# Kernel optimization log

Measured on AMD Instinct MI355X. Metric: run time of the kernel, lower is better.

Reference implementation:

```python
import jax, jax.numpy as jnp
import numpy as np

BLOCK = 256


def setup_inputs() -> dict:
    key = jax.random.key(0)
    ks = jax.random.split(key, 6)
    b, n, hid = 2, 4096, 2048
    h, d = 16, 128
    x = jax.random.normal(ks[0], (b, n, hid), dtype=jnp.float32)
    slope_rate = jax.random.uniform(ks[1], (h, 1, 1), dtype=jnp.float32)
    Wqkv = jax.random.normal(ks[2], (3 * h * d, hid), dtype=jnp.float32) * 0.02
    Wg = jax.random.normal(ks[3], (h * d, hid), dtype=jnp.float32) * 0.02
    norm_w = jnp.ones((h * d,), dtype=jnp.float32)
    Wo = jax.random.normal(ks[4], (hid, h * d), dtype=jnp.float32) * 0.02
    return {"x": x, "slope_rate": slope_rate, "Wqkv": Wqkv, "Wg": Wg, "norm_w": norm_w, "Wo": Wo}


def reference(x, slope_rate, Wqkv, Wg, norm_w, Wo):
    b, n, hid = x.shape
    h = slope_rate.shape[0]
    d = Wqkv.shape[0] // (3 * h)
    nb = n // BLOCK

    qkv = jax.nn.silu(x @ Wqkv.T).reshape(b, n, h, 3 * d)
    q, k, v = jnp.split(qkv, 3, axis=-1)           # each (b, n, h, d)
    # -> (b, h, n, d)
    q = q.transpose(0, 2, 1, 3)
    k = k.transpose(0, 2, 1, 3)
    v = v.transpose(0, 2, 1, 3)

    s = slope_rate.astype(jnp.float32)             # (h, 1, 1)
    arr = jnp.arange(1, BLOCK + 1, dtype=jnp.float32)
    q_decay = jnp.exp(-s * arr[:, None])           # (h, BLOCK, 1)
    k_decay = jnp.exp(-s * (BLOCK - arr[:, None])) # (h, BLOCK, 1)
    idx = arr[:, None] - arr[None, :]              # (BLOCK, BLOCK)
    diag_decay = jnp.where(idx >= 0, jnp.exp(-s * idx), 0.0)  # (h, BLOCK, BLOCK)
    block_decay = jnp.exp(-s * BLOCK)              # (h, 1, 1)

    # chunk into blocks: (nb, b, h, BLOCK, d)
    def chunk(t):
        return t.reshape(b, h, nb, BLOCK, d).transpose(2, 0, 1, 3, 4)
    qc, kc, vc = chunk(q), chunk(k), chunk(v)

    def step(kv, qkv_blk):
        qi, ki, vi = qkv_blk
        # inter-block: decayed query against running kv state
        out_nd = jnp.einsum('bhmd,bhde->bhme', qi * q_decay, kv)
        # intra-block: decay-masked quadratic attention
        qk = jnp.einsum('bhmd,bhnd->bhmn', qi, ki) * diag_decay
        out_d = jnp.einsum('bhmn,bhne->bhme', qk, vi)
        kv_new = block_decay * kv + jnp.einsum('bhmd,bhme->bhde', ki * k_decay, vi)
        return kv_new, out_nd + out_d

    kv0 = jnp.zeros((b, h, d, d), dtype=jnp.float32)
    _, out_blocks = jax.lax.scan(step, kv0, (qc, kc, vc))  # (nb, b, h, BLOCK, d)

    out = out_blocks.transpose(1, 2, 0, 3, 4).reshape(b, h, n, d)
    out = out.transpose(0, 2, 1, 3).reshape(b, n, h * d)  # b n (h d)

    # RMSNorm
    eps = jnp.finfo(jnp.float32).eps
    rms = jax.lax.rsqrt(jnp.mean(out * out, axis=-1, keepdims=True) + eps)
    out = out * rms * norm_w

    gate = jax.nn.sigmoid(x @ Wg.T)
    return (gate * out) @ Wo.T
```

## Files before the change

kernel.cpp:

```cpp
#include <hip/hip_runtime.h>
#include <stdint.h>

typedef __attribute__((ext_vector_type(8))) short short8;
typedef __attribute__((ext_vector_type(4))) float f32x4;

#define DEV static __device__ __forceinline__

DEV float b2f(unsigned short u) {
  unsigned x = ((unsigned)u) << 16;
  return __builtin_bit_cast(float, x);
}
DEV unsigned short f2b(float f) {
  unsigned x = __builtin_bit_cast(unsigned, f);
  return (unsigned short)((x + 0x7fffu + ((x >> 16) & 1u)) >> 16);
}
DEV void gload16(const unsigned short* g, unsigned short* l) {
  __builtin_amdgcn_global_load_lds((const __attribute__((address_space(1))) void*)g,
                                   (__attribute__((address_space(3))) void*)l, 16, 0, 0);
}
#define MFMA(a, b, c) __builtin_amdgcn_mfma_f32_16x16x32_bf16(a, b, c, 0, 0, 0)

__global__ void k_f2b(const float* __restrict__ in, unsigned short* __restrict__ out, long n) {
  long i = ((long)blockIdx.x * blockDim.x + threadIdx.x) * 4;
  long stride = (long)gridDim.x * blockDim.x * 4;
  for (; i < n; i += stride) {
    float4 f = *(const float4*)(in + i);
    ushort4 o;
    o.x = f2b(f.x); o.y = f2b(f.y); o.z = f2b(f.z); o.w = f2b(f.w);
    *(ushort4*)(out + i) = o;
  }
}

template <int MODE>
__global__ __launch_bounds__(512, 2) void k_gemm(
    const unsigned short* __restrict__ A, const unsigned short* __restrict__ B0,
    const unsigned short* __restrict__ B1,
    unsigned short* __restrict__ o_q, unsigned short* __restrict__ o_k,
    unsigned short* __restrict__ o_v, unsigned short* __restrict__ o_g,
    float* __restrict__ o_f) {
  const int K = 2048, NT = 32;
  __shared__ unsigned short sm[65536];
  int tid = threadIdx.x, w = tid >> 6, lane = tid & 63;
  int wm = w >> 2, wn = w & 3;
  int l15 = lane & 15, l4 = lane >> 4;
  int xcd = blockIdx.x & 7, sub = blockIdx.x >> 3;
  int tm = xcd * 4 + (sub & 3), tn = sub >> 2;
  int brow = tm << 8, bcol = tn << 8;
  const unsigned short* Ab = A + (size_t)brow * K;
  const unsigned short* Bb = (MODE == 1 || bcol < 6144) ? (B0 + (size_t)bcol * K)
                                                        : (B1 + (size_t)(bcol - 6144) * K);
  f32x4 acc[8][4];
#pragma unroll
  for (int m = 0; m < 8; m++)
#pragma unroll
    for (int n = 0; n < 4; n++) acc[m][n] = (f32x4)0.f;

  auto stageU = [&](int TT, int s) {
    if (TT >= NT) return;
    unsigned short* lb = sm + (TT & 1) * 32768 + s * 8192;
    int kt = TT << 6;
    const unsigned short* gb = (s & 1) ? Bb : Ab;
    int ro = (s >> 1) << 7;
#pragma unroll
    for (int i = 0; i < 2; ++i) {
      int c = i * 512 + tid;
      int pos = c >> 3, pb = c & 7;
      gload16(gb + (size_t)(ro + pos) * K + kt + ((pb ^ (pos & 7)) << 3), lb + c * 8);
    }
  };

  stageU(0, 0); stageU(0, 1); stageU(0, 3); stageU(0, 2);
  asm volatile("s_waitcnt vmcnt(2)" ::: "memory");
  __builtin_amdgcn_s_barrier();
  asm volatile("" ::: "memory");

  int bslot = (wn >> 1) ? 3 : 1;
  int bposb = (wn & 1) * 64;

  for (int T = 0; T < NT; ++T) {
    const unsigned short* bufb = sm + (T & 1) * 32768;
    const unsigned short* Bbase = bufb + bslot * 8192;
    short8 bfr[4][2], af[4][2];
#pragma unroll
    for (int ni = 0; ni < 4; ++ni) {
      int pos = bposb + ni * 16 + l15;
#pragma unroll
      for (int ks = 0; ks < 2; ++ks)
        bfr[ni][ks] = *(const short8*)(Bbase + pos * 64 + (((ks * 4 + l4) ^ (pos & 7)) << 3));
    }
#pragma unroll
    for (int mi = 0; mi < 4; ++mi) {
      int pos = wm * 64 + mi * 16 + l15;
#pragma unroll
      for (int ks = 0; ks < 2; ++ks)
        af[mi][ks] = *(const short8*)(bufb + pos * 64 + (((ks * 4 + l4) ^ (pos & 7)) << 3));
    }
    stageU(T + 1, 0); stageU(T + 1, 1); stageU(T + 1, 3);
    __builtin_amdgcn_s_setprio(1);
#pragma unroll
    for (int mi = 0; mi < 4; ++mi)
#pragma unroll
      for (int ni = 0; ni < 4; ++ni)
#pragma unroll
        for (int ks = 0; ks < 2; ++ks) acc[mi][ni] = MFMA(af[mi][ks], bfr[ni][ks], acc[mi][ni]);
    __builtin_amdgcn_s_setprio(0);
    asm volatile("s_waitcnt vmcnt(6)" ::: "memory");
    __builtin_amdgcn_s_barrier();
    asm volatile("" ::: "memory");
    const unsigned short* A1 = bufb + 2 * 8192;
#pragma unroll
    for (int mi = 0; mi < 4; ++mi) {
      int pos = wm * 64 + mi * 16 + l15;
#pragma unroll
      for (int ks = 0; ks < 2; ++ks)
        af[mi][ks] = *(const short8*)(A1 + pos * 64 + (((ks * 4 + l4) ^ (pos & 7)) << 3));
    }
    stageU(T + 1, 2);
    __builtin_amdgcn_s_setprio(1);
#pragma unroll
    for (int mi = 0; mi < 4; ++mi)
#pragma unroll
      for (int ni = 0; ni < 4; ++ni)
#pragma unroll
        for (int ks = 0; ks < 2; ++ks)
          acc[4 + mi][ni] = MFMA(af[mi][ks], bfr[ni][ks], acc[4 + mi][ni]);
    __builtin_amdgcn_s_setprio(0);
    asm volatile("s_waitcnt vmcnt(2)" ::: "memory");
    __builtin_amdgcn_s_barrier();
    asm volatile("" ::: "memory");
  }

#pragma unroll
  for (int mf = 0; mf < 8; ++mf)
#pragma unroll
    for (int r = 0; r < 4; ++r) {
      int row = brow + (mf >> 2) * 128 + wm * 64 + (mf & 3) * 16 + l4 * 4 + r;
#pragma unroll
      for (int ni = 0; ni < 4; ++ni) {
        int col = bcol + wn * 64 + ni * 16 + l15;
        float v = acc[mf][ni][r];
        if (MODE == 0) {
          if (col < 6144) {
            float sv = v / (1.f + __expf(-v));
            int h = col / 384, dd = col - h * 384;
            int b = row >> 12, t = row & 4095;
            size_t base = ((size_t)(b * 16 + h) * 4096 + t) * 128;
            if (dd < 128) o_q[base + dd] = f2b(sv);
            else if (dd < 256) o_k[base + dd - 128] = f2b(sv);
            else o_v[base + dd - 256] = f2b(sv);
          } else {
            float gv = 1.f / (1.f + __expf(-v));
            o_g[(size_t)row * 2048 + (col - 6144)] = f2b(gv);
          }
        } else {
          o_f[(size_t)row * 2048 + col] = v;
        }
      }
    }
}

__global__ __launch_bounds__(256) void k_kvblk(const unsigned short* __restrict__ kk,
                                               const unsigned short* __restrict__ vv,
                                               const float* __restrict__ slope,
                                               unsigned short* __restrict__ kvT) {
  int gid = blockIdx.x;
  int bh = gid >> 4, blk = gid & 15;
  float s = slope[bh & 15];
  __shared__ unsigned short kT[128][72];
  __shared__ unsigned short vT[128][72];
  int tid = threadIdx.x, w = tid >> 6, lane = tid & 63;
  int wrow = (w >> 1) * 64, wcol = (w & 1) * 64;
  f32x4 acc[4][4];
#pragma unroll
  for (int m = 0; m < 4; m++)
#pragma unroll
    for (int n = 0; n < 4; n++) acc[m][n] = (f32x4)0.f;
  const unsigned short* kb = kk + ((size_t)bh * 4096 + blk * 256) * 128;
  const unsigned short* vb = vv + ((size_t)bh * 4096 + blk * 256) * 128;
  int tt = tid & 63, c0 = (tid >> 6) * 32;
  for (int tc = 0; tc < 4; ++tc) {
    __syncthreads();
    int tg = tc * 64 + tt;
    float kd = __expf(-s * (float)(255 - tg));
#pragma unroll
    for (int g = 0; g < 4; ++g) {
      int c = c0 + g * 8;
      short8 k8 = *(const short8*)(kb + (size_t)tg * 128 + c);
      short8 v8 = *(const short8*)(vb + (size_t)tg * 128 + c);
#pragma unroll
      for (int j = 0; j < 8; ++j) {
        kT[c + j][tt] = f2b(b2f((unsigned short)k8[j]) * kd);
        vT[c + j][tt] = (unsigned short)v8[j];
      }
    }
    __syncthreads();
#pragma unroll
    for (int kx = 0; kx < 64; kx += 32) {
      int ko = kx + (lane >> 4) * 8;
      short8 af[4], bfr[4];
#pragma unroll
      for (int m = 0; m < 4; m++) af[m] = *(const short8*)&vT[wrow + m * 16 + (lane & 15)][ko];
#pragma unroll
      for (int n = 0; n < 4; n++) bfr[n] = *(const short8*)&kT[wcol + n * 16 + (lane & 15)][ko];
#pragma unroll
      for (int m = 0; m < 4; m++)
#pragma unroll
        for (int n = 0; n < 4; n++) acc[m][n] = MFMA(af[m], bfr[n], acc[m][n]);
    }
  }
  unsigned short* op = kvT + (size_t)gid * 16384;
#pragma unroll
  for (int m = 0; m < 4; m++)
#pragma unroll
    for (int r = 0; r < 4; r++) {
      int e = wrow + m * 16 + (lane >> 4) * 4 + r;
#pragma unroll
      for (int n = 0; n < 4; n++) {
        int d = wcol + n * 16 + (lane & 15);
        op[e * 128 + d] = f2b(acc[m][n][r]);
      }
    }
}

__global__ void k_scan(unsigned short* kvT, const float* __restrict__ slope) {
  int gid = blockIdx.x;
  int bh = gid >> 6;
  int eo = (gid & 63) * 256 + threadIdx.x;
  float s = slope[bh & 15];
  float bd = __expf(-s * 256.f);
  float st = 0.f;
  size_t base = (size_t)bh * 16 * 16384 + eo;
#pragma unroll
  for (int i = 0; i < 16; ++i) {
    unsigned short c = kvT[base + (size_t)i * 16384];
    kvT[base + (size_t)i * 16384] = f2b(st);
    st = bd * st + b2f(c);
  }
}

__global__ __launch_bounds__(256) void k_attn(const unsigned short* __restrict__ q,
                                              const unsigned short* __restrict__ kk,
                                              const unsigned short* __restrict__ vv,
                                              const unsigned short* __restrict__ kvT,
                                              const float* __restrict__ slope,
                                              unsigned short* __restrict__ attn) {
  int gid = blockIdx.x;
  int hf = gid & 1, blk = (gid >> 1) & 15, bh = gid >> 5;
  float s = slope[bh & 15];
  __shared__ unsigned short k_sh[64][136];
  __shared__ unsigned short vT_sh[128][72];
  __shared__ unsigned short s_sh[4][32][72];
  int tid = threadIdx.x, w = tid >> 6, lane = tid & 63;
  int mm0 = hf * 128 + w * 32;
  const unsigned short* qb = q + ((size_t)bh * 4096 + blk * 256) * 128;
  const unsigned short* kvb = kvT + (size_t)(bh * 16 + blk) * 16384;
  f32x4 acc[2][8];
#pragma unroll
  for (int m = 0; m < 2; m++)
#pragma unroll
    for (int n = 0; n < 8; n++) acc[m][n] = (f32x4)0.f;
#pragma unroll
  for (int kx = 0; kx < 128; kx += 32) {
    int ko = kx + (lane >> 4) * 8;
    short8 af[2], bfr[8];
#pragma unroll
    for (int mi = 0; mi < 2; mi++)
      af[mi] = *(const short8*)(qb + (size_t)(mm0 + mi * 16 + (lane & 15)) * 128 + ko);
#pragma unroll
    for (int ni = 0; ni < 8; ni++)
      bfr[ni] = *(const short8*)(kvb + (size_t)(ni * 16 + (lane & 15)) * 128 + ko);
#pragma unroll
    for (int mi = 0; mi < 2; mi++)
#pragma unroll
      for (int ni = 0; ni < 8; ni++) acc[mi][ni] = MFMA(af[mi], bfr[ni], acc[mi][ni]);
  }
#pragma unroll
  for (int mi = 0; mi < 2; mi++)
#pragma unroll
    for (int r = 0; r < 4; r++) {
      float qd = __expf(-s * (float)(mm0 + mi * 16 + (lane >> 4) * 4 + r + 1));
#pragma unroll
      for (int ni = 0; ni < 8; ni++) acc[mi][ni][r] *= qd;
    }
  int nchunk = 2 * (hf + 1);
  for (int tc = 0; tc < nchunk; ++tc) {
    __syncthreads();
    {
      int t2 = tid >> 2, c = (tid & 3) * 32;
      const unsigned short* kp = kk + ((size_t)bh * 4096 + blk * 256 + tc * 64 + t2) * 128 + c;
#pragma unroll
      for (int g = 0; g < 4; ++g) *(short8*)&k_sh[t2][c + g * 8] = *(const short8*)(kp + g * 8);
    }
    {
      int t2 = tid & 63, e0 = (tid >> 6) * 32;
      const unsigned short* vp = vv + ((size_t)bh * 4096 + blk * 256 + tc * 64 + t2) * 128 + e0;
#pragma unroll
      for (int g = 0; g < 4; ++g) {
        short8 v8 = *(const short8*)(vp + g * 8);
#pragma unroll
        for (int j = 0; j < 8; ++j) vT_sh[e0 + g * 8 + j][t2] = (unsigned short)v8[j];
      }
    }
    __syncthreads();
    if (tc * 64 <= mm0 + 31) {
      f32x4 sa[2][4];
#pragma unroll
      for (int m = 0; m < 2; m++)
#pragma unroll
        for (int n = 0; n < 4; n++) sa[m][n] = (f32x4)0.f;
#pragma unroll
      for (int kx = 0; kx < 128; kx += 32) {
        int ko = kx + (lane >> 4) * 8;
        short8 af[2], bfr[4];
#pragma unroll
        for (int mi = 0; mi < 2; mi++)
          af[mi] = *(const short8*)(qb + (size_t)(mm0 + mi * 16 + (lane & 15)) * 128 + ko);
#pragma unroll
        for (int ni = 0; ni < 4; ni++) bfr[ni] = *(const short8*)&k_sh[ni * 16 + (lane & 15)][ko];
#pragma unroll
        for (int mi = 0; mi < 2; mi++)
#pragma unroll
          for (int ni = 0; ni < 4; ni++) sa[mi][ni] = MFMA(af[mi], bfr[ni], sa[mi][ni]);
      }
#pragma unroll
      for (int mi = 0; mi < 2; mi++)
#pragma unroll
        for (int ni = 0; ni < 4; ni++)
#pragma unroll
          for (int r = 0; r < 4; r++) {
            int mm = mm0 + mi * 16 + (lane >> 4) * 4 + r;
            int ttg = tc * 64 + ni * 16 + (lane & 15);
            int diff = mm - ttg;
            float val = (diff >= 0) ? sa[mi][ni][r] * __expf(-s * (float)diff) : 0.f;
            s_sh[w][mi * 16 + (lane >> 4) * 4 + r][ni * 16 + (lane & 15)] = f2b(val);
          }
#pragma unroll
      for (int k2 = 0; k2 < 64; k2 += 32) {
        int ko2 = k2 + (lane >> 4) * 8;
        short8 a2[2];
#pragma unroll
        for (int mi = 0; mi < 2; mi++)
          a2[mi] = *(const short8*)&s_sh[w][mi * 16 + (lane & 15)][ko2];
#pragma unroll
        for (int ni = 0; ni < 8; ni++) {
          short8 b2 = *(const short8*)&vT_sh[ni * 16 + (lane & 15)][ko2];
#pragma unroll
          for (int mi = 0; mi < 2; mi++) acc[mi][ni] = MFMA(a2[mi], b2, acc[mi][ni]);
        }
      }
    }
  }
  int b = bh >> 4, h = bh & 15;
#pragma unroll
  for (int mi = 0; mi < 2; mi++)
#pragma unroll
    for (int r = 0; r < 4; r++) {
      int mm = mm0 + mi * 16 + (lane >> 4) * 4 + r;
      size_t rowp = ((size_t)b * 4096 + blk * 256 + mm) * 2048 + h * 128;
#pragma unroll
      for (int ni = 0; ni < 8; ni++) attn[rowp + ni * 16 + (lane & 15)] = f2b(acc[mi][ni][r]);
    }
}

__global__ __launch_bounds__(256) void k_norm(const unsigned short* __restrict__ attn,
                                              const unsigned short* __restrict__ gate,
                                              const float* __restrict__ nw,
                                              unsigned short* __restrict__ y) {
  int row = blockIdx.x;
  int tid = threadIdx.x, w = tid >> 6, lane = tid & 63;
  const unsigned short* ap = attn + (size_t)row * 2048 + tid * 8;
  const unsigned short* gp = gate + (size_t)row * 2048 + tid * 8;
  short8 a8 = *(const short8*)ap;
  float vals[8];
  float ss = 0.f;
#pragma unroll
  for (int j = 0; j < 8; ++j) {
    vals[j] = b2f((unsigned short)a8[j]);
    ss += vals[j] * vals[j];
  }
#pragma unroll
  for (int off = 32; off > 0; off >>= 1) ss += __shfl_down(ss, off, 64);
  __shared__ float red[4];
  if (lane == 0) red[w] = ss;
  __syncthreads();
  float tot = red[0] + red[1] + red[2] + red[3];
  float rms = rsqrtf(tot * (1.f / 2048.f) + 1.1920929e-07f);
  short8 g8 = *(const short8*)gp;
  short8 o;
#pragma unroll
  for (int j = 0; j < 8; ++j)
    o[j] = (short)f2b(vals[j] * rms * nw[tid * 8 + j] * b2f((unsigned short)g8[j]));
  *(short8*)(y + (size_t)row * 2048 + tid * 8) = o;
}

extern "C" void kernel_launch(void* const* d_in, const int* in_sizes, int n_in, void* d_out,
                              int out_size, void* d_ws, size_t ws_size, hipStream_t stream) {
  const float* x = (const float*)d_in[0];
  const float* slope = (const float*)d_in[1];
  const float* Wqkv = (const float*)d_in[2];
  const float* Wg = (const float*)d_in[3];
  const float* nw = (const float*)d_in[4];
  const float* Wo = (const float*)d_in[5];
  float* out = (float*)d_out;

  unsigned short* q = (unsigned short*)d_ws;
  unsigned short* k = q + 16777216;
  unsigned short* v = k + 16777216;
  unsigned short* gate = v + 16777216;
  unsigned short* xb = gate + 16777216;
  unsigned short* wqkvb = xb + 16777216;
  unsigned short* wgb = wqkvb + 12582912;
  unsigned short* wob = wgb + 4194304;
  unsigned short* kvT = wob + 4194304;
  unsigned short* attn = wqkvb;
  unsigned short* y = xb;

  k_f2b<<<2048, 256, 0, stream>>>(x, xb, 16777216L);
  k_f2b<<<2048, 256, 0, stream>>>(Wqkv, wqkvb, 12582912L);
  k_f2b<<<1024, 256, 0, stream>>>(Wg, wgb, 4194304L);
  k_f2b<<<1024, 256, 0, stream>>>(Wo, wob, 4194304L);

  k_gemm<0><<<1024, 512, 0, stream>>>(xb, wqkvb, wgb, q, k, v, gate, nullptr);
  k_kvblk<<<512, 256, 0, stream>>>(k, v, slope, kvT);
  k_scan<<<2048, 256, 0, stream>>>(kvT, slope);
  k_attn<<<1024, 256, 0, stream>>>(q, k, v, kvT, slope, attn);
  k_norm<<<8192, 256, 0, stream>>>(attn, gate, nw, y);
  k_gemm<1><<<256, 512, 0, stream>>>(y, wob, nullptr, nullptr, nullptr, nullptr, nullptr, out);
}
```

Before: 505.4 us.

## Deepen GEMM LDS pipeline to two tiles ahead with quadrant-split MFMA phases

Restructures the bf16 GEMM main loop. It prefetches K-tiles two iterations ahead into the double-buffered LDS, refilling each slot as soon as its fragments are in registers. The MFMA work is split into four quadrant phases separated by barriers, with LDS fragment reads and global-to-LDS loads interleaved between them. Out-of-range stages now reload the last tile instead of returning, so vmcnt counts stay uniform. The aim is to hide global-load latency and overlap LDS reads with MFMA, at the cost of more barriers per iteration and redundant tail loads.

```diff
diff --git a/kernel.cpp b/kernel.cpp
--- a/kernel.cpp
+++ b/kernel.cpp
@@ -19,6 +19,10 @@
                                    (__attribute__((address_space(3))) void*)l, 16, 0, 0);
 }
 #define MFMA(a, b, c) __builtin_amdgcn_mfma_f32_16x16x32_bf16(a, b, c, 0, 0, 0)
+#define BARRIER                          \
+  asm volatile("" ::: "memory");         \
+  __builtin_amdgcn_s_barrier();          \
+  asm volatile("" ::: "memory")
 
 __global__ void k_f2b(const float* __restrict__ in, unsigned short* __restrict__ out, long n) {
   long i = ((long)blockIdx.x * blockDim.x + threadIdx.x) * 4;
@@ -56,9 +60,9 @@
     for (int n = 0; n < 4; n++) acc[m][n] = (f32x4)0.f;
 
   auto stageU = [&](int TT, int s) {
-    if (TT >= NT) return;
+    int tsrc = TT < NT ? TT : NT - 1;
     unsigned short* lb = sm + (TT & 1) * 32768 + s * 8192;
-    int kt = TT << 6;
+    int kt = tsrc << 6;
     const unsigned short* gb = (s & 1) ? Bb : Ab;
     int ro = (s >> 1) << 7;
 #pragma unroll
@@ -70,64 +74,70 @@
   };
 
   stageU(0, 0); stageU(0, 1); stageU(0, 3); stageU(0, 2);
-  asm volatile("s_waitcnt vmcnt(2)" ::: "memory");
-  __builtin_amdgcn_s_barrier();
-  asm volatile("" ::: "memory");
-
-  int bslot = (wn >> 1) ? 3 : 1;
-  int bposb = (wn & 1) * 64;
+  stageU(1, 0); stageU(1, 1); stageU(1, 3);
+  asm volatile("s_waitcnt vmcnt(8)" ::: "memory");
+  BARRIER;
+
+  const int bslot = (wn >> 1) ? 3 : 1;
+  const int bposb = (wn & 1) * 64;
 
   for (int T = 0; T < NT; ++T) {
     const unsigned short* bufb = sm + (T & 1) * 32768;
-    const unsigned short* Bbase = bufb + bslot * 8192;
-    short8 bfr[4][2], af[4][2];
-#pragma unroll
-    for (int ni = 0; ni < 4; ++ni) {
-      int pos = bposb + ni * 16 + l15;
-#pragma unroll
-      for (int ks = 0; ks < 2; ++ks)
-        bfr[ni][ks] = *(const short8*)(Bbase + pos * 64 + (((ks * 4 + l4) ^ (pos & 7)) << 3));
-    }
-#pragma unroll
-    for (int mi = 0; mi < 4; ++mi) {
-      int pos = wm * 64 + mi * 16 + l15;
-#pragma unroll
-      for (int ks = 0; ks < 2; ++ks)
-        af[mi][ks] = *(const short8*)(bufb + pos * 64 + (((ks * 4 + l4) ^ (pos & 7)) << 3));
-    }
-    stageU(T + 1, 0); stageU(T + 1, 1); stageU(T + 1, 3);
-    __builtin_amdgcn_s_setprio(1);
-#pragma unroll
-    for (int mi = 0; mi < 4; ++mi)
-#pragma unroll
-      for (int ni = 0; ni < 4; ++ni)
-#pragma unroll
-        for (int ks = 0; ks < 2; ++ks) acc[mi][ni] = MFMA(af[mi][ks], bfr[ni][ks], acc[mi][ni]);
-    __builtin_amdgcn_s_setprio(0);
-    asm volatile("s_waitcnt vmcnt(6)" ::: "memory");
-    __builtin_amdgcn_s_barrier();
-    asm volatile("" ::: "memory");
-    const unsigned short* A1 = bufb + 2 * 8192;
-#pragma unroll
-    for (int mi = 0; mi < 4; ++mi) {
-      int pos = wm * 64 + mi * 16 + l15;
-#pragma unroll
-      for (int ks = 0; ks < 2; ++ks)
-        af[mi][ks] = *(const short8*)(A1 + pos * 64 + (((ks * 4 + l4) ^ (pos & 7)) << 3));
-    }
+    const unsigned short* Bslot = bufb + bslot * 8192;
+    short8 af[4][2], bfr[2][2][2];
+
+    auto ldA = [&](const unsigned short* base) {
+#pragma unroll
+      for (int mi = 0; mi < 4; ++mi) {
+        int pos = wm * 64 + mi * 16 + l15;
+#pragma unroll
+        for (int ks = 0; ks < 2; ++ks)
+          af[mi][ks] = *(const short8*)(base + pos * 64 + (((ks * 4 + l4) ^ (pos & 7)) << 3));
+      }
+    };
+    auto ldB = [&](int nh) {
+#pragma unroll
+      for (int nj = 0; nj < 2; ++nj) {
+        int pos = bposb + nh * 32 + nj * 16 + l15;
+#pragma unroll
+        for (int ks = 0; ks < 2; ++ks)
+          bfr[nh][nj][ks] = *(const short8*)(Bslot + pos * 64 + (((ks * 4 + l4) ^ (pos & 7)) << 3));
+      }
+    };
+    auto mfmaQ = [&](int mh, int nh) {
+      __builtin_amdgcn_s_setprio(1);
+#pragma unroll
+      for (int mi = 0; mi < 4; ++mi)
+#pragma unroll
+        for (int nj = 0; nj < 2; ++nj)
+#pragma unroll
+          for (int ks = 0; ks < 2; ++ks)
+            acc[mh * 4 + mi][nh * 2 + nj] =
+                MFMA(af[mi][ks], bfr[nh][nj][ks], acc[mh * 4 + mi][nh * 2 + nj]);
+      __builtin_amdgcn_s_setprio(0);
+    };
+
+    ldA(bufb);
+    ldB(0);
     stageU(T + 1, 2);
-    __builtin_amdgcn_s_setprio(1);
-#pragma unroll
-    for (int mi = 0; mi < 4; ++mi)
-#pragma unroll
-      for (int ni = 0; ni < 4; ++ni)
-#pragma unroll
-        for (int ks = 0; ks < 2; ++ks)
-          acc[4 + mi][ni] = MFMA(af[mi][ks], bfr[ni][ks], acc[4 + mi][ni]);
-    __builtin_amdgcn_s_setprio(0);
-    asm volatile("s_waitcnt vmcnt(2)" ::: "memory");
-    __builtin_amdgcn_s_barrier();
-    asm volatile("" ::: "memory");
+    BARRIER;
+    mfmaQ(0, 0);
+    BARRIER;
+    ldB(1);
+    stageU(T + 2, 0);
+    BARRIER;
+    mfmaQ(0, 1);
+    asm volatile("s_waitcnt vmcnt(10)" ::: "memory");
+    BARRIER;
+    ldA(bufb + 2 * 8192);
+    stageU(T + 2, 1);
+    stageU(T + 2, 3);
+    BARRIER;
+    mfmaQ(1, 1);
+    BARRIER;
+    mfmaQ(1, 0);
+    asm volatile("s_waitcnt vmcnt(8)" ::: "memory");
+    BARRIER;
   }
 
 #pragma unroll
```

Measured after the change: 520.8 us. 1.03x slower.
